# Performance work log

Hardware: AMD Instinct MI355X
Metric: run time of the kernel (lower is better)

The kernel has to match this reference:

```python
import jax, jax.numpy as jnp
import numpy as np

D_MODEL = 1024
N_HEADS = 16
D_HEAD = D_MODEL // N_HEADS
BLOCK = 128
B, T = 2, 2048


def setup_inputs() -> dict:
    key = jax.random.key(0)
    ks = jax.random.split(key, 5)
    x = jax.random.normal(ks[0], (B, T, D_MODEL), dtype=jnp.float32)
    def init_w(k):
        # nn.Linear default init scale ~ 1/sqrt(fan_in)
        return jax.random.normal(k, (D_MODEL, D_MODEL), dtype=jnp.float32) / np.sqrt(D_MODEL).astype(np.float32)
    return {
        "x": x,
        "Wq": init_w(ks[1]),
        "Wk": init_w(ks[2]),
        "Wv": init_w(ks[3]),
        "Wo": init_w(ks[4]),
    }


def _flash_attention(Q, K, V, block_size, scale):
    """Online-softmax tiled attention over kv blocks (causal). Q,K,V: (B,H,T,d)."""
    Bb, H, Tt, d = Q.shape
    n_blocks = Tt // block_size
    # (n_blocks, B, H, block, d) so scan streams kv tiles
    Kb = K.reshape(Bb, H, n_blocks, block_size, d).transpose(2, 0, 1, 3, 4)
    Vb = V.reshape(Bb, H, n_blocks, block_size, d).transpose(2, 0, 1, 3, 4)
    starts = jnp.arange(n_blocks) * block_size
    q_pos = jnp.arange(Tt)

    def step(carry, xs):
        m, l, acc = carry
        kb, vb, st = xs
        # scores: (B,H,T,block)
        scores = scale * jnp.einsum('bhtd,bhsd->bhts', Q, kb)
        kv_pos = st + jnp.arange(block_size)
        future = kv_pos[None, :] > q_pos[:, None]          # (T, block)
        scores = jnp.where(future[None, None], -jnp.inf, scores)
        m_new = jnp.maximum(m, jnp.max(scores, axis=-1, keepdims=True))
        p = jnp.exp(scores - m_new)
        corr = jnp.exp(m - m_new)
        l = corr * l + jnp.sum(p, axis=-1, keepdims=True)
        acc = corr * acc + jnp.einsum('bhts,bhsd->bhtd', p, vb)
        return (m_new, l, acc), None

    m0 = jnp.full((Bb, H, Tt, 1), -jnp.inf, dtype=jnp.float32)
    l0 = jnp.zeros((Bb, H, Tt, 1), dtype=jnp.float32)
    a0 = jnp.zeros((Bb, H, Tt, d), dtype=jnp.float32)
    (m, l, acc), _ = jax.lax.scan(step, (m0, l0, a0), (Kb, Vb, starts))
    return acc / jnp.maximum(l, 1e-12)


def reference(x, Wq, Wk, Wv, Wo):
    Bx, Tx, _ = x.shape
    scale = 1.0 / np.sqrt(D_HEAD).astype(np.float32)
    def proj(W):  # nn.Linear: y = x @ W.T
        y = jnp.einsum('btm,nm->btn', x, W)
        return y.reshape(Bx, Tx, N_HEADS, D_HEAD).transpose(0, 2, 1, 3)
    Q, K, V = proj(Wq), proj(Wk), proj(Wv)
    O = _flash_attention(Q.astype(jnp.float32), K.astype(jnp.float32), V.astype(jnp.float32), BLOCK, scale)
    O = O.astype(x.dtype).transpose(0, 2, 1, 3).reshape(Bx, Tx, D_MODEL)
    return jnp.einsum('btm,nm->btn', O, Wo)
```

## Files before the change

### kernel.cpp

```cpp
#include <hip/hip_runtime.h>
#include <hip/hip_bf16.h>

typedef __attribute__((ext_vector_type(8))) short short8;
typedef __attribute__((ext_vector_type(4))) float f32x4;
typedef __attribute__((ext_vector_type(2))) unsigned int uint2v;
typedef __attribute__((ext_vector_type(4))) unsigned int uint4v;
typedef unsigned short u16;

#define MFMA_BF16(a, b, c) __builtin_amdgcn_mfma_f32_16x16x32_bf16(a, b, c, 0, 0, 0)

#define T_SEQ 2048
#define DMODEL 1024
#define NHEADS 16
#define DHEAD 64
#define NEG_BIG (-30000.0f)
#define QSCALE 0.1803368801111f

#define EXP2(x) exp2f(x)

__device__ __forceinline__ unsigned bfr(unsigned u) {
  return (u + 0x7fffu + ((u >> 16) & 1u)) >> 16;
}
__device__ __forceinline__ uint4v ld8bf(const float* __restrict__ p) {
  const uint4v a = *(const uint4v*)p;
  const uint4v b = *(const uint4v*)(p + 4);
  uint4v r;
  r[0] = bfr(a[0]) | (bfr(a[1]) << 16);
  r[1] = bfr(a[2]) | (bfr(a[3]) << 16);
  r[2] = bfr(b[0]) | (bfr(b[1]) << 16);
  r[3] = bfr(b[2]) | (bfr(b[3]) << 16);
  return r;
}
__device__ __forceinline__ u16 f2bf(float f) {
  unsigned u = __float_as_uint(f);
  u += 0x7fffu + ((u >> 16) & 1u);
  return (u16)(u >> 16);
}
__device__ __forceinline__ void gld16(const u16* g, u16* l) {
  __builtin_amdgcn_global_load_lds(
      (const __attribute__((address_space(1))) unsigned int*)g,
      (__attribute__((address_space(3))) unsigned int*)l, 16, 0, 0);
}

__global__ __launch_bounds__(256) void cvt_all(
    const float* __restrict__ x, const float* __restrict__ wq,
    const float* __restrict__ wk, const float* __restrict__ wv,
    const float* __restrict__ wo, u16* __restrict__ xh, u16* __restrict__ wqh,
    u16* __restrict__ wkh, u16* __restrict__ wvh, u16* __restrict__ woh) {
  int bi = blockIdx.x;
  const float* s;
  u16* d;
  size_t base;
  if (bi < 2048) {
    s = x; d = xh; base = (size_t)bi * 2048;
  } else {
    int k = (bi - 2048) >> 9;
    int r = (bi - 2048) & 511;
    s = (k == 0) ? wq : (k == 1) ? wk : (k == 2) ? wv : wo;
    d = (k == 0) ? wqh : (k == 1) ? wkh : (k == 2) ? wvh : woh;
    base = (size_t)r * 2048;
  }
  size_t i = base + (size_t)threadIdx.x * 8;
  *(uint4v*)&d[i] = ld8bf(&s[i]);
}

__global__ __launch_bounds__(256) void gemm_qkv(
    const u16* __restrict__ X, const u16* __restrict__ Wq,
    const u16* __restrict__ Wk, const u16* __restrict__ Wv,
    u16* __restrict__ Qo, u16* __restrict__ Ko, u16* __restrict__ Vo) {
  __shared__ __attribute__((aligned(16))) u16 As[128 * 32];
  __shared__ __attribute__((aligned(16))) u16 Bs[128 * 32];
  const int tid = threadIdx.x, lane = tid & 63, w = tid >> 6;
  const int wm = (w >> 1) * 64, wn = (w & 1) * 64;
  const int lrow = lane & 15;
  const int quad = lane >> 4;
  const int lk = quad << 3;
  const int lq = quad << 2;
  const int mBase = blockIdx.x * 128, nBase = blockIdx.y * 128;
  const u16* Bt = (blockIdx.z == 0) ? Wq : (blockIdx.z == 1) ? Wk : Wv;
  u16* D = (blockIdx.z == 0) ? Qo : (blockIdx.z == 1) ? Ko : Vo;
  const float scale = (blockIdx.z == 0) ? QSCALE : 1.0f;
  const int vz = (blockIdx.z == 2);

  f32x4 acc[4][4];
#pragma unroll
  for (int mi = 0; mi < 4; mi++)
#pragma unroll
    for (int ni = 0; ni < 4; ni++) acc[mi][ni] = (f32x4)0.0f;

  for (int k0 = 0; k0 < 1024; k0 += 32) {
    __syncthreads();
#pragma unroll
    for (int i = 0; i < 2; i++) {
      int c = i * 256 + tid;
      int r = c >> 2, kk = (c & 3) << 3;
      gld16(&X[(size_t)(mBase + r) * 1024 + k0 + kk], &As[c * 8]);
      gld16(&Bt[(size_t)(nBase + r) * 1024 + k0 + kk], &Bs[c * 8]);
    }
    __syncthreads();
    short8 af[4], bf[4];
#pragma unroll
    for (int mi = 0; mi < 4; mi++)
      af[mi] = *(const short8*)&As[(wm + mi * 16 + lrow) * 32 + lk];
#pragma unroll
    for (int ni = 0; ni < 4; ni++)
      bf[ni] = *(const short8*)&Bs[(wn + ni * 16 + lrow) * 32 + lk];
    if (!vz) {
#pragma unroll
      for (int mi = 0; mi < 4; mi++)
#pragma unroll
        for (int ni = 0; ni < 4; ni++)
          acc[mi][ni] = MFMA_BF16(bf[ni], af[mi], acc[mi][ni]);
    } else {
#pragma unroll
      for (int mi = 0; mi < 4; mi++)
#pragma unroll
        for (int ni = 0; ni < 4; ni++)
          acc[mi][ni] = MFMA_BF16(af[mi], bf[ni], acc[mi][ni]);
    }
  }

  if (!vz) {
#pragma unroll
    for (int mi = 0; mi < 4; mi++) {
      int m = mBase + wm + mi * 16 + lrow;
      int b = m >> 11, t = m & 2047;
#pragma unroll
      for (int ni = 0; ni < 4; ni++) {
        int n0 = nBase + wn + ni * 16 + lq;
        int h = n0 >> 6, dd = n0 & 63;
        uint2v pk;
        pk[0] = (unsigned)f2bf(acc[mi][ni][0] * scale) |
                ((unsigned)f2bf(acc[mi][ni][1] * scale) << 16);
        pk[1] = (unsigned)f2bf(acc[mi][ni][2] * scale) |
                ((unsigned)f2bf(acc[mi][ni][3] * scale) << 16);
        *(uint2v*)&D[(((size_t)(b * NHEADS + h)) * T_SEQ + t) * DHEAD + dd] = pk;
      }
    }
  } else {
#pragma unroll
    for (int mi = 0; mi < 4; mi++) {
      int m0 = mBase + wm + mi * 16 + lq;
      int b = m0 >> 11, t0 = m0 & 2047;
#pragma unroll
      for (int ni = 0; ni < 4; ni++) {
        int n = nBase + wn + ni * 16 + lrow;
        int h = n >> 6, dd = n & 63;
        uint2v pk;
        pk[0] = (unsigned)f2bf(acc[mi][ni][0]) |
                ((unsigned)f2bf(acc[mi][ni][1]) << 16);
        pk[1] = (unsigned)f2bf(acc[mi][ni][2]) |
                ((unsigned)f2bf(acc[mi][ni][3]) << 16);
        *(uint2v*)&D[((size_t)((b * NHEADS + h) * DHEAD + dd)) * T_SEQ + t0] = pk;
      }
    }
  }
}

__global__ __launch_bounds__(256) void attn_snake(
    const u16* __restrict__ Qg, const u16* __restrict__ Kg,
    const u16* __restrict__ Vtg, u16* __restrict__ Ob) {
  __shared__ __attribute__((aligned(16))) u16 smem[26624];
  u16* Ks = smem;
  u16* Vt = smem + 9216;
  u16* Ps = smem + 17920;
  u16* Qs = Ps;

  const int tid = threadIdx.x;
  const int w = tid >> 6, lane = tid & 63;
  const int lrow = lane & 15;
  const int quad = lane >> 4;
  const int lk = quad << 3;
  const int q_local = w * 16 + lrow;

  const int bh = blockIdx.x;
  const int j = blockIdx.y;
  const int b = bh >> 4, h = bh & 15;
  const u16* Qp = Qg + (size_t)bh * T_SEQ * DHEAD;
  const u16* Kp = Kg + (size_t)bh * T_SEQ * DHEAD;
  const u16* Vp = Vtg + (size_t)bh * DHEAD * T_SEQ;

#pragma unroll
  for (int p = 0; p < 2; p++) {
    const int qt = p ? (31 - j) : j;
    const int qb = qt * 64;

    __syncthreads();
#pragma unroll
    for (int i = 0; i < 2; i++) {
      int c = i * 256 + tid;
      int r = c >> 3, kk = (c & 7) << 3;
      *(uint4v*)&Qs[r * 72 + kk] =
          *(const uint4v*)&Qp[(size_t)(qb + r) * DHEAD + kk];
    }
    __syncthreads();
    short8 qf[2];
#pragma unroll
    for (int ks = 0; ks < 2; ks++)
      qf[ks] = *(const short8*)&Qs[q_local * 72 + ks * 32 + lk];

    float mst = NEG_BIG, lst = 0.f;
    f32x4 oacc[4];
#pragma unroll
    for (int nd = 0; nd < 4; nd++) oacc[nd] = (f32x4)0.0f;

    const int ntiles = (qt >> 1) + 1;
    for (int kt = 0; kt < ntiles; kt++) {
      const int kvb = kt * 128;
      __syncthreads();
#pragma unroll
      for (int i = 0; i < 4; i++) {
        int c = i * 256 + tid;
        int r = c >> 3, kk = (c & 7) << 3;
        *(uint4v*)&Ks[r * 72 + kk] =
            *(const uint4v*)&Kp[(size_t)(kvb + r) * DHEAD + kk];
      }
#pragma unroll
      for (int i = 0; i < 4; i++) {
        int c = i * 256 + tid;
        int d = c >> 4, kk = (c & 15) << 3;
        *(uint4v*)&Vt[d * 136 + kk] =
            *(const uint4v*)&Vp[(size_t)d * T_SEQ + kvb + kk];
      }
      __syncthreads();

      f32x4 s[8];
#pragma unroll
      for (int kvt = 0; kvt < 8; kvt++) {
        f32x4 a = (f32x4)0.0f;
#pragma unroll
        for (int ks = 0; ks < 2; ks++) {
          short8 kf = *(const short8*)&Ks[(kvt * 16 + lrow) * 72 + ks * 32 + lk];
          a = MFMA_BF16(kf, qf[ks], a);
        }
        s[kvt] = a;
      }

      if (kt == ntiles - 1) {
#pragma unroll
        for (int kvt = 0; kvt < 8; kvt++)
#pragma unroll
          for (int r = 0; r < 4; r++)
            if (kvb + kvt * 16 + quad * 4 + r > qb + q_local)
              s[kvt][r] = NEG_BIG;
      }

      float mx = s[0][0];
#pragma unroll
      for (int kvt = 0; kvt < 8; kvt++)
#pragma unroll
        for (int r = 0; r < 4; r++) mx = fmaxf(mx, s[kvt][r]);
      mx = fmaxf(mx, __shfl_xor(mx, 16));
      mx = fmaxf(mx, __shfl_xor(mx, 32));
      float mn = fmaxf(mst, mx);
      float corr = EXP2(mst - mn);
      mst = mn;
      float ls = 0.f;
#pragma unroll
      for (int kvt = 0; kvt < 8; kvt++)
#pragma unroll
        for (int r = 0; r < 4; r++) {
          float pv = EXP2(s[kvt][r] - mn);
          s[kvt][r] = pv;
          ls += pv;
        }
      ls += __shfl_xor(ls, 16);
      ls += __shfl_xor(ls, 32);
      lst = corr * lst + ls;
#pragma unroll
      for (int nd = 0; nd < 4; nd++) oacc[nd] *= corr;

#pragma unroll
      for (int kvt = 0; kvt < 8; kvt++) {
        uint2v pk;
        pk[0] = (__float_as_uint(s[kvt][0]) >> 16) |
                (__float_as_uint(s[kvt][1]) & 0xffff0000u);
        pk[1] = (__float_as_uint(s[kvt][2]) >> 16) |
                (__float_as_uint(s[kvt][3]) & 0xffff0000u);
        *(uint2v*)&Ps[q_local * 136 + kvt * 16 + quad * 4] = pk;
      }

#pragma unroll
      for (int ks = 0; ks < 4; ks++) {
        short8 pf = *(const short8*)&Ps[q_local * 136 + ks * 32 + lk];
#pragma unroll
        for (int nd = 0; nd < 4; nd++) {
          short8 vf = *(const short8*)&Vt[(nd * 16 + lrow) * 136 + ks * 32 + lk];
          oacc[nd] = MFMA_BF16(vf, pf, oacc[nd]);
        }
      }
    }

    float inv = 1.f / lst;
    size_t rowbase = ((size_t)(b * T_SEQ + qb + q_local)) * DMODEL + h * DHEAD;
#pragma unroll
    for (int nd = 0; nd < 4; nd++) {
      uint2v pk;
      pk[0] = (unsigned)f2bf(oacc[nd][0] * inv) |
              ((unsigned)f2bf(oacc[nd][1] * inv) << 16);
      pk[1] = (unsigned)f2bf(oacc[nd][2] * inv) |
              ((unsigned)f2bf(oacc[nd][3] * inv) << 16);
      *(uint2v*)&Ob[rowbase + nd * 16 + quad * 4] = pk;
    }
  }
}

__global__ __launch_bounds__(256) void gemm_out_bf(const u16* __restrict__ O,
                                                   const u16* __restrict__ Wo,
                                                   float* __restrict__ Out) {
  __shared__ __attribute__((aligned(16))) u16 As[128 * 32];
  __shared__ __attribute__((aligned(16))) u16 Bs[128 * 32];
  const int tid = threadIdx.x, lane = tid & 63, w = tid >> 6;
  const int wm = (w >> 1) * 64, wn = (w & 1) * 64;
  const int lrow = lane & 15;
  const int quad = lane >> 4;
  const int lk = quad << 3;
  const int mBase = blockIdx.x * 128, nBase = blockIdx.y * 128;

  f32x4 acc[4][4];
#pragma unroll
  for (int mi = 0; mi < 4; mi++)
#pragma unroll
    for (int ni = 0; ni < 4; ni++) acc[mi][ni] = (f32x4)0.0f;

  for (int k0 = 0; k0 < 1024; k0 += 32) {
    __syncthreads();
#pragma unroll
    for (int i = 0; i < 2; i++) {
      int c = i * 256 + tid;
      int r = c >> 2, kk = (c & 3) << 3;
      gld16(&O[(size_t)(mBase + r) * 1024 + k0 + kk], &As[c * 8]);
      gld16(&Wo[(size_t)(nBase + r) * 1024 + k0 + kk], &Bs[c * 8]);
    }
    __syncthreads();
    short8 af[4], bf[4];
#pragma unroll
    for (int mi = 0; mi < 4; mi++)
      af[mi] = *(const short8*)&As[(wm + mi * 16 + lrow) * 32 + lk];
#pragma unroll
    for (int ni = 0; ni < 4; ni++)
      bf[ni] = *(const short8*)&Bs[(wn + ni * 16 + lrow) * 32 + lk];
#pragma unroll
    for (int mi = 0; mi < 4; mi++)
#pragma unroll
      for (int ni = 0; ni < 4; ni++)
        acc[mi][ni] = MFMA_BF16(bf[ni], af[mi], acc[mi][ni]);
  }
#pragma unroll
  for (int mi = 0; mi < 4; mi++) {
    int m = mBase + wm + mi * 16 + lrow;
#pragma unroll
    for (int ni = 0; ni < 4; ni++) {
      int n0 = nBase + wn + ni * 16 + (quad << 2);
      *(f32x4*)&Out[(size_t)m * DMODEL + n0] = acc[mi][ni];
    }
  }
}

extern "C" void kernel_launch(void* const* d_in, const int* in_sizes, int n_in,
                              void* d_out, int out_size, void* d_ws,
                              size_t ws_size, hipStream_t stream) {
  const float* x = (const float*)d_in[0];
  const float* Wq = (const float*)d_in[1];
  const float* Wk = (const float*)d_in[2];
  const float* Wv = (const float*)d_in[3];
  const float* Wo = (const float*)d_in[4];
  float* out = (float*)d_out;

  u16* xh = (u16*)d_ws;
  u16* wqh = xh + 4194304;
  u16* wkh = wqh + 1048576;
  u16* wvh = wkh + 1048576;
  u16* woh = wvh + 1048576;
  u16* Q = woh + 1048576;
  u16* K = Q + 4194304;
  u16* V = K + 4194304;
  u16* O = V + 4194304;

  cvt_all<<<dim3(4096), 256, 0, stream>>>(x, Wq, Wk, Wv, Wo, xh, wqh, wkh, wvh, woh);
  gemm_qkv<<<dim3(32, 8, 3), 256, 0, stream>>>(xh, wqh, wkh, wvh, Q, K, V);
  attn_snake<<<dim3(32, 16), 256, 0, stream>>>(Q, K, V, O);
  gemm_out_bf<<<dim3(32, 8), 256, 0, stream>>>(O, woh, out);
}
```

Baseline: 203.9 us.

## Use padded 64-deep GEMM tiles and register-prefetch K/V tiles in attention

Both GEMMs drop the direct global-to-LDS loads for register-staged loads into padded 72-stride shared tiles, use a K step of 64, and swap the MFMA operand order. Their epilogues now write scalar elements instead of packed vectors. The attention kernel prefetches the next K/V tile into registers while the current tile is computed, so global latency overlaps with MFMA work. The cost is more register pressure, LDS use and less coalesced stores in the GEMM epilogues.

```diff
diff --git a/kernel.cpp b/kernel.cpp
--- a/kernel.cpp
+++ b/kernel.cpp
@@ -35,11 +35,6 @@
   unsigned u = __float_as_uint(f);
   u += 0x7fffu + ((u >> 16) & 1u);
   return (u16)(u >> 16);
-}
-__device__ __forceinline__ void gld16(const u16* g, u16* l) {
-  __builtin_amdgcn_global_load_lds(
-      (const __attribute__((address_space(1))) unsigned int*)g,
-      (__attribute__((address_space(3))) unsigned int*)l, 16, 0, 0);
 }
 
 __global__ __launch_bounds__(256) void cvt_all(
@@ -68,8 +63,8 @@
     const u16* __restrict__ X, const u16* __restrict__ Wq,
     const u16* __restrict__ Wk, const u16* __restrict__ Wv,
     u16* __restrict__ Qo, u16* __restrict__ Ko, u16* __restrict__ Vo) {
-  __shared__ __attribute__((aligned(16))) u16 As[128 * 32];
-  __shared__ __attribute__((aligned(16))) u16 Bs[128 * 32];
+  __shared__ __attribute__((aligned(16))) u16 As[128 * 72];
+  __shared__ __attribute__((aligned(16))) u16 Bs[128 * 72];
   const int tid = threadIdx.x, lane = tid & 63, w = tid >> 6;
   const int wm = (w >> 1) * 64, wn = (w & 1) * 64;
   const int lrow = lane & 15;
@@ -88,30 +83,27 @@
 #pragma unroll
     for (int ni = 0; ni < 4; ni++) acc[mi][ni] = (f32x4)0.0f;
 
-  for (int k0 = 0; k0 < 1024; k0 += 32) {
-    __syncthreads();
-#pragma unroll
-    for (int i = 0; i < 2; i++) {
+  for (int k0 = 0; k0 < 1024; k0 += 64) {
+    __syncthreads();
+#pragma unroll
+    for (int i = 0; i < 4; i++) {
       int c = i * 256 + tid;
-      int r = c >> 2, kk = (c & 3) << 3;
-      gld16(&X[(size_t)(mBase + r) * 1024 + k0 + kk], &As[c * 8]);
-      gld16(&Bt[(size_t)(nBase + r) * 1024 + k0 + kk], &Bs[c * 8]);
-    }
-    __syncthreads();
-    short8 af[4], bf[4];
-#pragma unroll
-    for (int mi = 0; mi < 4; mi++)
-      af[mi] = *(const short8*)&As[(wm + mi * 16 + lrow) * 32 + lk];
-#pragma unroll
-    for (int ni = 0; ni < 4; ni++)
-      bf[ni] = *(const short8*)&Bs[(wn + ni * 16 + lrow) * 32 + lk];
-    if (!vz) {
+      int r = c >> 3, kk = (c & 7) << 3;
+      *(uint4v*)&As[r * 72 + kk] =
+          *(const uint4v*)&X[(size_t)(mBase + r) * 1024 + k0 + kk];
+      *(uint4v*)&Bs[r * 72 + kk] =
+          *(const uint4v*)&Bt[(size_t)(nBase + r) * 1024 + k0 + kk];
+    }
+    __syncthreads();
+#pragma unroll
+    for (int kh = 0; kh < 2; kh++) {
+      short8 af[4], bf[4];
 #pragma unroll
       for (int mi = 0; mi < 4; mi++)
-#pragma unroll
-        for (int ni = 0; ni < 4; ni++)
-          acc[mi][ni] = MFMA_BF16(bf[ni], af[mi], acc[mi][ni]);
-    } else {
+        af[mi] = *(const short8*)&As[(wm + mi * 16 + lrow) * 72 + kh * 32 + lk];
+#pragma unroll
+      for (int ni = 0; ni < 4; ni++)
+        bf[ni] = *(const short8*)&Bs[(wn + ni * 16 + lrow) * 72 + kh * 32 + lk];
 #pragma unroll
       for (int mi = 0; mi < 4; mi++)
 #pragma unroll
@@ -122,21 +114,19 @@
 
   if (!vz) {
 #pragma unroll
-    for (int mi = 0; mi < 4; mi++) {
-      int m = mBase + wm + mi * 16 + lrow;
-      int b = m >> 11, t = m & 2047;
-#pragma unroll
-      for (int ni = 0; ni < 4; ni++) {
-        int n0 = nBase + wn + ni * 16 + lq;
-        int h = n0 >> 6, dd = n0 & 63;
-        uint2v pk;
-        pk[0] = (unsigned)f2bf(acc[mi][ni][0] * scale) |
-                ((unsigned)f2bf(acc[mi][ni][1] * scale) << 16);
-        pk[1] = (unsigned)f2bf(acc[mi][ni][2] * scale) |
-                ((unsigned)f2bf(acc[mi][ni][3] * scale) << 16);
-        *(uint2v*)&D[(((size_t)(b * NHEADS + h)) * T_SEQ + t) * DHEAD + dd] = pk;
-      }
-    }
+    for (int mi = 0; mi < 4; mi++)
+#pragma unroll
+      for (int r = 0; r < 4; r++) {
+        int m = mBase + wm + mi * 16 + lq + r;
+        int b = m >> 11, t = m & 2047;
+#pragma unroll
+        for (int ni = 0; ni < 4; ni++) {
+          int n = nBase + wn + ni * 16 + lrow;
+          int h = n >> 6, dd = n & 63;
+          D[(((size_t)(b * NHEADS + h)) * T_SEQ + t) * DHEAD + dd] =
+              f2bf(acc[mi][ni][r] * scale);
+        }
+      }
   } else {
 #pragma unroll
     for (int mi = 0; mi < 4; mi++) {
@@ -180,10 +170,25 @@
   const u16* Kp = Kg + (size_t)bh * T_SEQ * DHEAD;
   const u16* Vp = Vtg + (size_t)bh * DHEAD * T_SEQ;
 
+  int rk[4], ok[4], dv[4], ov[4];
+#pragma unroll
+  for (int i = 0; i < 4; i++) {
+    int c = i * 256 + tid;
+    rk[i] = c >> 3; ok[i] = (c & 7) << 3;
+    dv[i] = c >> 4; ov[i] = (c & 15) << 3;
+  }
+
 #pragma unroll
   for (int p = 0; p < 2; p++) {
     const int qt = p ? (31 - j) : j;
     const int qb = qt * 64;
+
+    uint4v kpre[4], vpre[4];
+#pragma unroll
+    for (int i = 0; i < 4; i++) {
+      kpre[i] = *(const uint4v*)&Kp[(size_t)rk[i] * DHEAD + ok[i]];
+      vpre[i] = *(const uint4v*)&Vp[(size_t)dv[i] * T_SEQ + ov[i]];
+    }
 
     __syncthreads();
 #pragma unroll
@@ -206,24 +211,23 @@
 
     const int ntiles = (qt >> 1) + 1;
     for (int kt = 0; kt < ntiles; kt++) {
+      __syncthreads();
+#pragma unroll
+      for (int i = 0; i < 4; i++) {
+        *(uint4v*)&Ks[rk[i] * 72 + ok[i]] = kpre[i];
+        *(uint4v*)&Vt[dv[i] * 136 + ov[i]] = vpre[i];
+      }
+      __syncthreads();
+      if (kt + 1 < ntiles) {
+        const int kvb2 = (kt + 1) * 128;
+#pragma unroll
+        for (int i = 0; i < 4; i++) {
+          kpre[i] = *(const uint4v*)&Kp[(size_t)(kvb2 + rk[i]) * DHEAD + ok[i]];
+          vpre[i] = *(const uint4v*)&Vp[(size_t)dv[i] * T_SEQ + kvb2 + ov[i]];
+        }
+      }
+
       const int kvb = kt * 128;
-      __syncthreads();
-#pragma unroll
-      for (int i = 0; i < 4; i++) {
-        int c = i * 256 + tid;
-        int r = c >> 3, kk = (c & 7) << 3;
-        *(uint4v*)&Ks[r * 72 + kk] =
-            *(const uint4v*)&Kp[(size_t)(kvb + r) * DHEAD + kk];
-      }
-#pragma unroll
-      for (int i = 0; i < 4; i++) {
-        int c = i * 256 + tid;
-        int d = c >> 4, kk = (c & 15) << 3;
-        *(uint4v*)&Vt[d * 136 + kk] =
-            *(const uint4v*)&Vp[(size_t)d * T_SEQ + kvb + kk];
-      }
-      __syncthreads();
-
       f32x4 s[8];
 #pragma unroll
       for (int kvt = 0; kvt < 8; kvt++) {
@@ -308,13 +312,14 @@
 __global__ __launch_bounds__(256) void gemm_out_bf(const u16* __restrict__ O,
                                                    const u16* __restrict__ Wo,
                                                    float* __restrict__ Out) {
-  __shared__ __attribute__((aligned(16))) u16 As[128 * 32];
-  __shared__ __attribute__((aligned(16))) u16 Bs[128 * 32];
+  __shared__ __attribute__((aligned(16))) u16 As[128 * 72];
+  __shared__ __attribute__((aligned(16))) u16 Bs[128 * 72];
   const int tid = threadIdx.x, lane = tid & 63, w = tid >> 6;
   const int wm = (w >> 1) * 64, wn = (w & 1) * 64;
   const int lrow = lane & 15;
   const int quad = lane >> 4;
   const int lk = quad << 3;
+  const int lq = quad << 2;
   const int mBase = blockIdx.x * 128, nBase = blockIdx.y * 128;
 
   f32x4 acc[4][4];
@@ -323,38 +328,43 @@
 #pragma unroll
     for (int ni = 0; ni < 4; ni++) acc[mi][ni] = (f32x4)0.0f;
 
-  for (int k0 = 0; k0 < 1024; k0 += 32) {
-    __syncthreads();
-#pragma unroll
-    for (int i = 0; i < 2; i++) {
+  for (int k0 = 0; k0 < 1024; k0 += 64) {
+    __syncthreads();
+#pragma unroll
+    for (int i = 0; i < 4; i++) {
       int c = i * 256 + tid;
-      int r = c >> 2, kk = (c & 3) << 3;
-      gld16(&O[(size_t)(mBase + r) * 1024 + k0 + kk], &As[c * 8]);
-      gld16(&Wo[(size_t)(nBase + r) * 1024 + k0 + kk], &Bs[c * 8]);
-    }
-    __syncthreads();
-    short8 af[4], bf[4];
-#pragma unroll
-    for (int mi = 0; mi < 4; mi++)
-      af[mi] = *(const short8*)&As[(wm + mi * 16 + lrow) * 32 + lk];
-#pragma unroll
-    for (int ni = 0; ni < 4; ni++)
-      bf[ni] = *(const short8*)&Bs[(wn + ni * 16 + lrow) * 32 + lk];
-#pragma unroll
-    for (int mi = 0; mi < 4; mi++)
+      int r = c >> 3, kk = (c & 7) << 3;
+      *(uint4v*)&As[r * 72 + kk] =
+          *(const uint4v*)&O[(size_t)(mBase + r) * 1024 + k0 + kk];
+      *(uint4v*)&Bs[r * 72 + kk] =
+          *(const uint4v*)&Wo[(size_t)(nBase + r) * 1024 + k0 + kk];
+    }
+    __syncthreads();
+#pragma unroll
+    for (int kh = 0; kh < 2; kh++) {
+      short8 af[4], bf[4];
+#pragma unroll
+      for (int mi = 0; mi < 4; mi++)
+        af[mi] = *(const short8*)&As[(wm + mi * 16 + lrow) * 72 + kh * 32 + lk];
 #pragma unroll
       for (int ni = 0; ni < 4; ni++)
-        acc[mi][ni] = MFMA_BF16(bf[ni], af[mi], acc[mi][ni]);
-  }
-#pragma unroll
-  for (int mi = 0; mi < 4; mi++) {
-    int m = mBase + wm + mi * 16 + lrow;
-#pragma unroll
-    for (int ni = 0; ni < 4; ni++) {
-      int n0 = nBase + wn + ni * 16 + (quad << 2);
-      *(f32x4*)&Out[(size_t)m * DMODEL + n0] = acc[mi][ni];
-    }
-  }
+        bf[ni] = *(const short8*)&Bs[(wn + ni * 16 + lrow) * 72 + kh * 32 + lk];
+#pragma unroll
+      for (int mi = 0; mi < 4; mi++)
+#pragma unroll
+        for (int ni = 0; ni < 4; ni++)
+          acc[mi][ni] = MFMA_BF16(af[mi], bf[ni], acc[mi][ni]);
+    }
+  }
+#pragma unroll
+  for (int mi = 0; mi < 4; mi++)
+#pragma unroll
+    for (int r = 0; r < 4; r++) {
+      int m = mBase + wm + mi * 16 + lq + r;
+#pragma unroll
+      for (int ni = 0; ni < 4; ni++)
+        Out[(size_t)m * DMODEL + nBase + wn + ni * 16 + lrow] = acc[mi][ni][r];
+    }
 }
 
 extern "C" void kernel_launch(void* const* d_in, const int* in_sizes, int n_in,
```

New measurement: 214.3 us. 5.1% more time.
